# Kernel tuning notes

Hardware: AMD Instinct MI355X
Metric: run time of the kernel (lower is better)

## Reference

```python
import jax, jax.numpy as jnp
import numpy as np

S, D, H, HD, FF = 4096, 1024, 16, 64, 4096  # seq, d_embed, heads, head_dim, hidden
EPS = 1e-6  # flax LayerNorm default epsilon


def layer_norm(x, scale, bias):
    mu = jnp.mean(x, axis=-1, keepdims=True)
    var = jnp.var(x, axis=-1, keepdims=True)
    return (x - mu) * jax.lax.rsqrt(var + EPS) * scale + bias


def rope(x):
    # x: [S, H, HD]; standard half-split rotary embedding, base 10000
    half = x.shape[-1] // 2
    freq = 1.0 / (10000.0 ** (jnp.arange(half, dtype=x.dtype) / half))  # [half]
    ang = jnp.arange(x.shape[0], dtype=x.dtype)[:, None] * freq          # [S, half]
    cos = jnp.cos(ang)[:, None, :]
    sin = jnp.sin(ang)[:, None, :]
    x1, x2 = x[..., :half], x[..., half:]
    return jnp.concatenate([x1 * cos - x2 * sin, x2 * cos + x1 * sin], axis=-1)


def setup_inputs() -> dict:
    key = jax.random.key(0)
    ks = jax.random.split(key, 8)
    s = 0.02
    return {
        "x": jax.random.normal(ks[0], (S, D), jnp.float32),
        "ln1_scale": jnp.ones((D,), jnp.float32), "ln1_bias": jnp.zeros((D,), jnp.float32),
        "ln2_scale": jnp.ones((D,), jnp.float32), "ln2_bias": jnp.zeros((D,), jnp.float32),
        "Wq": jax.random.normal(ks[1], (D, H, HD), jnp.float32) * s, "bq": jnp.zeros((H, HD), jnp.float32),
        "Wk": jax.random.normal(ks[2], (D, H, HD), jnp.float32) * s, "bk": jnp.zeros((H, HD), jnp.float32),
        "Wv": jax.random.normal(ks[3], (D, H, HD), jnp.float32) * s, "bv": jnp.zeros((H, HD), jnp.float32),
        "Wo": jax.random.normal(ks[4], (H, HD, D), jnp.float32) * s, "bo": jnp.zeros((D,), jnp.float32),
        "W1": jax.random.normal(ks[5], (D, FF), jnp.float32) * s, "b1": jnp.zeros((FF,), jnp.float32),
        "W2": jax.random.normal(ks[6], (FF, D), jnp.float32) * s, "b2": jnp.zeros((D,), jnp.float32),
    }


def reference(x, ln1_scale, ln1_bias, ln2_scale, ln2_bias, Wq, bq, Wk, bk, Wv, bv, Wo, bo, W1, b1, W2, b2):
    # Pre-LN attention block with RoPE fused into QK scores
    y = layer_norm(x, ln1_scale, ln1_bias)
    q = jnp.einsum('sd,dhc->shc', y, Wq) + bq  # [S,H,HD]
    k = jnp.einsum('sd,dhc->shc', y, Wk) + bk
    v = jnp.einsum('sd,dhc->shc', y, Wv) + bv
    q = rope(q)
    k = rope(k)
    scores = jnp.einsum('qhc,khc->hqk', q, k) / jnp.sqrt(jnp.asarray(HD, x.dtype))  # [H,S,S]
    p = jax.nn.softmax(scores, axis=-1)
    o = jnp.einsum('hqk,khc->qhc', p, v)                # [S,H,HD]
    attn_out = jnp.einsum('qhc,hcd->qd', o, Wo) + bo    # [S,D]
    x = x + attn_out
    # Pre-LN GELU MLP block
    y = layer_norm(x, ln2_scale, ln2_bias)
    y = jax.nn.gelu(y @ W1 + b1, approximate=False)
    x = x + (y @ W2 + b2)
    return x
```

## Files before the change

### kernel.cpp

```cpp
#include <hip/hip_runtime.h>
#include <hip/hip_bf16.h>
#include <math.h>

using bf16 = __hip_bfloat16;
typedef __attribute__((ext_vector_type(8))) short short8;
typedef __attribute__((ext_vector_type(4))) short s16x4;
typedef __attribute__((ext_vector_type(4))) float f32x4;

constexpr int S = 4096, D = 1024, H = 16, HD = 64, FF = 4096;

static __device__ __forceinline__ float tof(bf16 v) { return __bfloat162float(v); }
static __device__ __forceinline__ bf16 tob(float v) { return __float2bfloat16(v); }
static __device__ __forceinline__ short tobs(float v) {
    bf16 h = __float2bfloat16(v);
    return *reinterpret_cast<short*>(&h);
}
static __device__ __forceinline__ unsigned pkbf16(float a, float b) {
    __hip_bfloat162 h = __float22bfloat162_rn(make_float2(a, b));
    return *reinterpret_cast<unsigned*>(&h);
}

#if __has_builtin(__builtin_amdgcn_exp2f)
#define EXP2(x) __builtin_amdgcn_exp2f(x)
#else
#define EXP2(x) exp2f(x)
#endif

static __device__ __forceinline__ f32x4 mfma16(short8 a, short8 b, f32x4 c) {
    return __builtin_amdgcn_mfma_f32_16x16x32_bf16(a, b, c, 0, 0, 0);
}
static __device__ __forceinline__ void stage16(const bf16* g, bf16* l) {
    __builtin_amdgcn_global_load_lds((__attribute__((address_space(1))) void*)g,
                                     (__attribute__((address_space(3))) void*)l, 16, 0, 0);
}

__global__ __launch_bounds__(256) void ln_kernel(const float* __restrict__ x,
                                                 const float* __restrict__ scale,
                                                 const float* __restrict__ bias,
                                                 bf16* __restrict__ y) {
    int row = blockIdx.x, t = threadIdx.x;
    const float* xr = x + (size_t)row * D;
    float v[4], s = 0.f, ss = 0.f;
#pragma unroll
    for (int i = 0; i < 4; ++i) {
        v[i] = xr[t + 256 * i];
        s += v[i]; ss += v[i] * v[i];
    }
    __shared__ float r0[256], r1[256];
    r0[t] = s; r1[t] = ss;
    __syncthreads();
    for (int off = 128; off; off >>= 1) {
        if (t < off) { r0[t] += r0[t + off]; r1[t] += r1[t + off]; }
        __syncthreads();
    }
    float mu  = r0[0] * (1.f / D);
    float var = r1[0] * (1.f / D) - mu * mu;
    float inv = rsqrtf(var + 1e-6f);
    bf16* yr = y + (size_t)row * D;
#pragma unroll
    for (int i = 0; i < 4; ++i) {
        int c = t + 256 * i;
        yr[c] = tob((v[i] - mu) * inv * scale[c] + bias[c]);
    }
}

__global__ __launch_bounds__(256) void wtrans_all(
    const float* __restrict__ Wq, const float* __restrict__ Wk,
    const float* __restrict__ Wv, const float* __restrict__ Wo,
    const float* __restrict__ W1, const float* __restrict__ W2,
    const float* __restrict__ bq, const float* __restrict__ bk,
    const float* __restrict__ bv,
    bf16* __restrict__ BTqkv, bf16* __restrict__ BTo,
    bf16* __restrict__ BT1, bf16* __restrict__ BT2, float* __restrict__ bqkv) {
    int id = blockIdx.x;
    if (id >= 12288) {
        int i = (id - 12288) * 256 + threadIdx.x;
        bqkv[i] = i < 1024 ? bq[i] : (i < 2048 ? bk[i - 1024] : bv[i - 2048]);
        return;
    }
    const float* W; bf16* dst; int K, N, local;
    if (id < 3072)      { int s = id >> 10; W = s == 0 ? Wq : (s == 1 ? Wk : Wv);
                          dst = BTqkv + (size_t)s * 1048576; K = 1024; N = 1024; local = id & 1023; }
    else if (id < 4096) { W = Wo; dst = BTo; K = 1024; N = 1024; local = id - 3072; }
    else if (id < 8192) { W = W1; dst = BT1; K = 1024; N = 4096; local = id - 4096; }
    else                { W = W2; dst = BT2; K = 4096; N = 1024; local = id - 8192; }
    int ls = (N == 4096) ? 7 : 5;
    int nt = (local & ((1 << ls) - 1)) << 5, kt = (local >> ls) << 5;
    __shared__ float t[32][33];
    int tid = threadIdx.x, r = tid >> 5, c = tid & 31;
#pragma unroll
    for (int p = 0; p < 4; ++p)
        t[r + p * 8][c] = W[(size_t)(kt + r + p * 8) * N + nt + c];
    __syncthreads();
#pragma unroll
    for (int p = 0; p < 4; ++p)
        dst[(size_t)(nt + r + p * 8) * K + kt + c] = tob(t[c][r + p * 8]);
}

#define EPI_RES  1
#define EPI_GELU 2
#define EPI_QKV  3

template <int EPI, int MT>
__global__ __launch_bounds__(256, MT == 128 ? 2 : 3) void gemm_bt(
    const bf16* __restrict__ A, const bf16* __restrict__ BT,
    const float* __restrict__ bias, const float* resid, void* out, void* out2,
    int M, int N, int K) {
    constexpr int NJ = (MT == 128) ? 4 : 2;
    __shared__ bf16 As[MT * 32];
    __shared__ bf16 Bs[128 * 32];
    const int tid = threadIdx.x;
    const int w = tid >> 6, lane = tid & 63;
    const int quad = lane >> 4, l16 = lane & 15;
    const int rowBase = blockIdx.y * MT, colBase = blockIdx.x * 128;
    const int wr = (MT == 128) ? (w >> 1) * 64 : 0;
    const int wc = (MT == 128) ? (w & 1) * 64 : w * 32;
    const int sr = lane >> 2, skb = (lane & 3) * 8;
    f32x4 acc[4][NJ] = {};
    for (int k0 = 0; k0 < K; k0 += 32) {
        __syncthreads();
        if (MT == 128) {
#pragma unroll
            for (int t = 0; t < 2; ++t) {
                int inst = w * 2 + t;
                int r = inst * 16 + sr;
                stage16(A  + (size_t)(rowBase + r) * K + k0 + skb, As + inst * 512);
                stage16(BT + (size_t)(colBase + r) * K + k0 + skb, Bs + inst * 512);
            }
        } else {
            stage16(A + (size_t)(rowBase + w * 16 + sr) * K + k0 + skb, As + w * 512);
#pragma unroll
            for (int t = 0; t < 2; ++t) {
                int inst = w + t * 4;
                stage16(BT + (size_t)(colBase + inst * 16 + sr) * K + k0 + skb, Bs + inst * 512);
            }
        }
        __syncthreads();
        const bf16* pa = As + (wr + l16) * 32 + quad * 8;
        const bf16* pb = Bs + (wc + l16) * 32 + quad * 8;
        short8 a[4], b[NJ];
#pragma unroll
        for (int i = 0; i < 4; ++i) a[i] = *(const short8*)(pa + i * 512);
#pragma unroll
        for (int j = 0; j < NJ; ++j) b[j] = *(const short8*)(pb + j * 512);
#pragma unroll
        for (int i = 0; i < 4; ++i)
#pragma unroll
            for (int j = 0; j < NJ; ++j) acc[i][j] = mfma16(a[i], b[j], acc[i][j]);
    }
    if (EPI == EPI_QKV) {
        bf16* QKVo = (bf16*)out;
        bf16* VTo  = (bf16*)out2;
        if (colBase >= 2048) {
#pragma unroll
            for (int j = 0; j < NJ; ++j) {
                int c = colBase + wc + j * 16 + l16;
                float bj = bias[c];
                size_t cc = (size_t)(c - 2048) * 4096;
#pragma unroll
                for (int i = 0; i < 4; ++i) {
                    int r0 = rowBase + wr + i * 16 + quad * 4;
                    s16x4 ov = {tobs(acc[i][j][0] + bj), tobs(acc[i][j][1] + bj),
                                tobs(acc[i][j][2] + bj), tobs(acc[i][j][3] + bj)};
                    *(s16x4*)(VTo + cc + r0) = ov;
                }
            }
        } else {
            const bool isq = colBase < 1024;
            const float qs = isq ? 0.125f * 1.44269504088896f : 1.f;
#pragma unroll
            for (int j2 = 0; j2 < 2; ++j2) {
                int dim = j2 * 16 + l16;
                float freq = __expf(-(float)dim * (9.210340371976184f / 32.f));
                int c1 = colBase + wc + j2 * 16 + l16, c2 = c1 + 32;
                float b1v = bias[c1], b2v = bias[c2];
#pragma unroll
                for (int i = 0; i < 4; ++i) {
#pragma unroll
                    for (int reg = 0; reg < 4; ++reg) {
                        int s = rowBase + wr + i * 16 + quad * 4 + reg;
                        float sn, cs;
                        sincosf((float)s * freq, &sn, &cs);
                        float x1 = acc[i][j2][reg] + b1v;
                        float x2 = acc[i][j2 + 2][reg] + b2v;
                        QKVo[(size_t)s * 3072 + c1] = tob((x1 * cs - x2 * sn) * qs);
                        QKVo[(size_t)s * 3072 + c2] = tob((x2 * cs + x1 * sn) * qs);
                    }
                }
            }
        }
    } else {
#pragma unroll
        for (int j = 0; j < NJ; ++j) {
            int c = colBase + wc + j * 16 + l16;
            float bj = bias[c];
#pragma unroll
            for (int i = 0; i < 4; ++i) {
                int r0 = rowBase + wr + i * 16 + quad * 4;
#pragma unroll
                for (int reg = 0; reg < 4; ++reg) {
                    size_t idx = (size_t)(r0 + reg) * N + c;
                    float val = acc[i][j][reg] + bj;
                    if (EPI == EPI_RES) {
                        ((float*)out)[idx] = val + resid[idx];
                    } else {
                        float g = 0.5f * val * (1.f + erff(val * 0.70710678118f));
                        ((bf16*)out)[idx] = tob(g);
                    }
                }
            }
        }
    }
}

__global__ __launch_bounds__(256, 4) void attn_kernel(const bf16* __restrict__ QKV,
                                                      const bf16* __restrict__ VT,
                                                      bf16* __restrict__ O) {
    const int h = blockIdx.x >> 6, qb = blockIdx.x & 63;
    const int w = threadIdx.x >> 6, lane = threadIdx.x & 63;
    const int quad = lane >> 4, l16 = lane & 15;
    const int q0w = qb * 64 + w * 16;
    const bf16* Qh = QKV + h * 64;
    const bf16* Kh = QKV + 1024 + h * 64;
    const bf16* Vh = VT + (size_t)h * 64 * 4096;

    __shared__ char smem[40960];
    bf16* Ks = (bf16*)(smem);
    bf16* Vs = (bf16*)(smem + 16384);
    char* Pb = smem + 32768 + w * 2048;

    const int sw = l16 & 7;
    const int rloc = lane >> 3, slot = lane & 7;
    const int schunk = (slot ^ rloc) * 8;
    const int row0 = 2 * w * 8 + rloc, row1 = (2 * w + 1) * 8 + rloc;
    const size_t kOff0 = (size_t)row0 * 3072 + schunk;
    const size_t kOff1 = (size_t)row1 * 3072 + schunk;
    const size_t vOff0 = (size_t)row0 * 4096 + schunk;
    const size_t vOff1 = (size_t)row1 * 4096 + schunk;

    short8 qf[2];
#pragma unroll
    for (int c = 0; c < 2; ++c)
        qf[c] = *(const short8*)(Qh + (size_t)(q0w + l16) * 3072 + c * 32 + quad * 8);

    const short ob = (l16 == 0) ? (short)0x3F80 : (short)0;
    const short8 ones8 = {ob, ob, ob, ob, ob, ob, ob, ob};

    f32x4 acc[4] = {};
    f32x4 accl = {};
    const f32x4 zero = {0.f, 0.f, 0.f, 0.f};

    auto stage = [&](int sel, int kt) {
        bf16* kd = Ks + sel * 4096 + 2 * w * 512;
        bf16* vd = Vs + sel * 4096 + 2 * w * 512;
        const bf16* kb = Kh + (size_t)kt * 3072;
        stage16(kb + kOff0, kd);
        stage16(kb + kOff1, kd + 512);
        stage16(Vh + vOff0 + kt, vd);
        stage16(Vh + vOff1 + kt, vd + 512);
    };
    auto compute = [&](int sel) {
        const bf16* Kt = Ks + sel * 4096;
        const bf16* Vt = Vs + sel * 4096;
        f32x4 st[4];
#pragma unroll
        for (int nt = 0; nt < 4; ++nt) {
            const bf16* kr = Kt + (nt * 16 + l16) * 64;
            short8 k0 = *(const short8*)(kr + ((quad ^ sw) * 8));
            short8 k1 = *(const short8*)(kr + (((quad + 4) ^ sw) * 8));
            st[nt] = mfma16(k1, qf[1], mfma16(k0, qf[0], zero));
        }
#pragma unroll
        for (int nt = 0; nt < 4; ++nt) {
            float e0 = EXP2(st[nt][0]), e1 = EXP2(st[nt][1]);
            float e2 = EXP2(st[nt][2]), e3 = EXP2(st[nt][3]);
            uint2 pk = {pkbf16(e0, e1), pkbf16(e2, e3)};
            *(uint2*)(Pb + l16 * 128 + (((nt * 2 + (quad >> 1)) ^ sw) * 16) + (quad & 1) * 8) = pk;
        }
        asm volatile("s_waitcnt lgkmcnt(0)" ::: "memory");
#pragma unroll
        for (int c = 0; c < 2; ++c) {
            short8 pB = *(const short8*)(Pb + l16 * 128 + (((c * 4 + quad) ^ sw) * 16));
            accl = mfma16(ones8, pB, accl);
#pragma unroll
            for (int vt = 0; vt < 4; ++vt) {
                short8 vf = *(const short8*)(Vt + (vt * 16 + l16) * 64 + (((c * 4 + quad) ^ sw) * 8));
                acc[vt] = mfma16(vf, pB, acc[vt]);
            }
        }
    };

    stage(0, 0);
    for (int kt = 0; kt < 4096; kt += 128) {
        __syncthreads();
        stage(1, kt + 64);
        compute(0);
        __syncthreads();
        if (kt + 128 < 4096) stage(0, kt + 128);
        compute(1);
    }

    float linv = 1.f / __shfl(accl[0], l16, 64);
#pragma unroll
    for (int vt = 0; vt < 4; ++vt) {
        s16x4 ov = {tobs(acc[vt][0] * linv), tobs(acc[vt][1] * linv),
                    tobs(acc[vt][2] * linv), tobs(acc[vt][3] * linv)};
        *(s16x4*)(O + (size_t)(q0w + l16) * 1024 + h * 64 + vt * 16 + quad * 4) = ov;
    }
}

extern "C" void kernel_launch(void* const* d_in, const int* in_sizes, int n_in,
                              void* d_out, int out_size, void* d_ws, size_t ws_size,
                              hipStream_t stream) {
    const float* x   = (const float*)d_in[0];
    const float* s1  = (const float*)d_in[1];
    const float* b1n = (const float*)d_in[2];
    const float* s2  = (const float*)d_in[3];
    const float* b2n = (const float*)d_in[4];
    const float* Wq  = (const float*)d_in[5];
    const float* bq  = (const float*)d_in[6];
    const float* Wk  = (const float*)d_in[7];
    const float* bk  = (const float*)d_in[8];
    const float* Wv  = (const float*)d_in[9];
    const float* bv  = (const float*)d_in[10];
    const float* Wo  = (const float*)d_in[11];
    const float* bo  = (const float*)d_in[12];
    const float* W1  = (const float*)d_in[13];
    const float* b1  = (const float*)d_in[14];
    const float* W2  = (const float*)d_in[15];
    const float* b2  = (const float*)d_in[16];

    char* ws = (char*)d_ws;
    bf16*  y     = (bf16*)(ws);
    bf16*  QKV   = (bf16*)(ws + (8ull  << 20));
    bf16*  o     = (bf16*)(ws + (32ull << 20));
    bf16*  hb    = (bf16*)(ws + (40ull << 20));
    bf16*  BTqkv = (bf16*)(ws + (40ull << 20));
    bf16*  BTo   = (bf16*)(ws + (46ull << 20));
    bf16*  VT    = (bf16*)(ws + (72ull << 20));
    bf16*  BT1   = (bf16*)(ws + (80ull << 20));
    bf16*  BT2   = (bf16*)(ws + (88ull << 20));
    float* bqkv  = (float*)(ws + (32ull << 20));
    float* x1    = (float*)d_out;

    wtrans_all<<<12300, 256, 0, stream>>>(Wq, Wk, Wv, Wo, W1, W2, bq, bk, bv,
                                          BTqkv, BTo, BT1, BT2, bqkv);

    ln_kernel<<<S, 256, 0, stream>>>(x, s1, b1n, y);

    gemm_bt<EPI_QKV, 128><<<dim3(24, 32), 256, 0, stream>>>(y, BTqkv, bqkv, nullptr, QKV, VT, S, 3072, D);

    attn_kernel<<<H * 64, 256, 0, stream>>>(QKV, VT, o);

    gemm_bt<EPI_RES, 64><<<dim3(8, 64), 256, 0, stream>>>(o, BTo, bo, x, x1, nullptr, S, D, D);

    ln_kernel<<<S, 256, 0, stream>>>(x1, s2, b2n, y);

    gemm_bt<EPI_GELU, 128><<<dim3(32, 32), 256, 0, stream>>>(y, BT1, b1, nullptr, hb, nullptr, S, FF, D);

    gemm_bt<EPI_RES, 64><<<dim3(8, 64), 256, 0, stream>>>(hb, BT2, b2, x1, d_out, nullptr, S, D, FF);
}
```

Measured before the change: 433.2 us.

## Split attention keys and FFN2 reduction into halves with merge kernels

The attention kernel now splits the key range into two halves per (head, 128-query block). Each wave handles two 16-query tiles, so every K/V fragment staged in shared memory is reused twice. It writes unnormalized fp32 partial outputs and row sums, which a new merge kernel adds and normalizes. The FFN2 GEMM gains a split-K mode over a z grid dimension that writes fp32 partials, and a second merge kernel sums them with the bias and residual. Q/K are also stored with a compact 2048 stride. The changes aim to raise parallelism and data reuse, but they add fp32 partial traffic and drop the attention kernel's double-buffered K/V staging.

```diff
diff --git a/kernel.cpp b/kernel.cpp
--- a/kernel.cpp
+++ b/kernel.cpp
@@ -100,12 +100,13 @@
 #define EPI_RES  1
 #define EPI_GELU 2
 #define EPI_QKV  3
+#define EPI_PART 4
 
 template <int EPI, int MT>
 __global__ __launch_bounds__(256, MT == 128 ? 2 : 3) void gemm_bt(
     const bf16* __restrict__ A, const bf16* __restrict__ BT,
     const float* __restrict__ bias, const float* resid, void* out, void* out2,
-    int M, int N, int K) {
+    int M, int N, int K, int kLen) {
     constexpr int NJ = (MT == 128) ? 4 : 2;
     __shared__ bf16 As[MT * 32];
     __shared__ bf16 Bs[128 * 32];
@@ -113,26 +114,27 @@
     const int w = tid >> 6, lane = tid & 63;
     const int quad = lane >> 4, l16 = lane & 15;
     const int rowBase = blockIdx.y * MT, colBase = blockIdx.x * 128;
+    const int kStart = blockIdx.z * kLen;
     const int wr = (MT == 128) ? (w >> 1) * 64 : 0;
     const int wc = (MT == 128) ? (w & 1) * 64 : w * 32;
     const int sr = lane >> 2, skb = (lane & 3) * 8;
     f32x4 acc[4][NJ] = {};
-    for (int k0 = 0; k0 < K; k0 += 32) {
+    for (int k0 = 0; k0 < kLen; k0 += 32) {
         __syncthreads();
         if (MT == 128) {
 #pragma unroll
             for (int t = 0; t < 2; ++t) {
                 int inst = w * 2 + t;
                 int r = inst * 16 + sr;
-                stage16(A  + (size_t)(rowBase + r) * K + k0 + skb, As + inst * 512);
-                stage16(BT + (size_t)(colBase + r) * K + k0 + skb, Bs + inst * 512);
+                stage16(A  + (size_t)(rowBase + r) * K + kStart + k0 + skb, As + inst * 512);
+                stage16(BT + (size_t)(colBase + r) * K + kStart + k0 + skb, Bs + inst * 512);
             }
         } else {
-            stage16(A + (size_t)(rowBase + w * 16 + sr) * K + k0 + skb, As + w * 512);
+            stage16(A + (size_t)(rowBase + w * 16 + sr) * K + kStart + k0 + skb, As + w * 512);
 #pragma unroll
             for (int t = 0; t < 2; ++t) {
                 int inst = w + t * 4;
-                stage16(BT + (size_t)(colBase + inst * 16 + sr) * K + k0 + skb, Bs + inst * 512);
+                stage16(BT + (size_t)(colBase + inst * 16 + sr) * K + kStart + k0 + skb, Bs + inst * 512);
             }
         }
         __syncthreads();
@@ -149,8 +151,8 @@
             for (int j = 0; j < NJ; ++j) acc[i][j] = mfma16(a[i], b[j], acc[i][j]);
     }
     if (EPI == EPI_QKV) {
-        bf16* QKVo = (bf16*)out;
-        bf16* VTo  = (bf16*)out2;
+        bf16* QKo = (bf16*)out;
+        bf16* VTo = (bf16*)out2;
         if (colBase >= 2048) {
 #pragma unroll
             for (int j = 0; j < NJ; ++j) {
@@ -183,8 +185,8 @@
                         sincosf((float)s * freq, &sn, &cs);
                         float x1 = acc[i][j2][reg] + b1v;
                         float x2 = acc[i][j2 + 2][reg] + b2v;
-                        QKVo[(size_t)s * 3072 + c1] = tob((x1 * cs - x2 * sn) * qs);
-                        QKVo[(size_t)s * 3072 + c2] = tob((x2 * cs + x1 * sn) * qs);
+                        QKo[(size_t)s * 2048 + c1] = tob((x1 * cs - x2 * sn) * qs);
+                        QKo[(size_t)s * 2048 + c2] = tob((x2 * cs + x1 * sn) * qs);
                     }
                 }
             }
@@ -193,7 +195,7 @@
 #pragma unroll
         for (int j = 0; j < NJ; ++j) {
             int c = colBase + wc + j * 16 + l16;
-            float bj = bias[c];
+            float bj = (EPI == EPI_PART) ? 0.f : bias[c];
 #pragma unroll
             for (int i = 0; i < 4; ++i) {
                 int r0 = rowBase + wr + i * 16 + quad * 4;
@@ -203,6 +205,8 @@
                     float val = acc[i][j][reg] + bj;
                     if (EPI == EPI_RES) {
                         ((float*)out)[idx] = val + resid[idx];
+                    } else if (EPI == EPI_PART) {
+                        ((float*)out)[(size_t)blockIdx.z * M * N + idx] = val;
                     } else {
                         float g = 0.5f * val * (1.f + erff(val * 0.70710678118f));
                         ((bf16*)out)[idx] = tob(g);
@@ -213,100 +217,131 @@
     }
 }
 
-__global__ __launch_bounds__(256, 4) void attn_kernel(const bf16* __restrict__ QKV,
+__global__ __launch_bounds__(256, 4) void attn_kernel(const bf16* __restrict__ QK,
                                                       const bf16* __restrict__ VT,
-                                                      bf16* __restrict__ O) {
-    const int h = blockIdx.x >> 6, qb = blockIdx.x & 63;
+                                                      float* __restrict__ Op,
+                                                      float* __restrict__ lp) {
+    const int bx = blockIdx.x;
+    const int h = bx >> 6, qb = (bx & 63) >> 1, kh = bx & 1;
     const int w = threadIdx.x >> 6, lane = threadIdx.x & 63;
     const int quad = lane >> 4, l16 = lane & 15;
-    const int q0w = qb * 64 + w * 16;
-    const bf16* Qh = QKV + h * 64;
-    const bf16* Kh = QKV + 1024 + h * 64;
+    const int q0w = qb * 128 + w * 32;
+    const bf16* Qh = QK + h * 64;
+    const bf16* Kh = QK + 1024 + h * 64;
     const bf16* Vh = VT + (size_t)h * 64 * 4096;
 
-    __shared__ char smem[40960];
+    __shared__ char smem[32768];
     bf16* Ks = (bf16*)(smem);
-    bf16* Vs = (bf16*)(smem + 16384);
-    char* Pb = smem + 32768 + w * 2048;
+    bf16* Vs = (bf16*)(smem + 8192);
+    char* Pw = smem + 16384 + w * 4096;
 
     const int sw = l16 & 7;
     const int rloc = lane >> 3, slot = lane & 7;
     const int schunk = (slot ^ rloc) * 8;
-    const int row0 = 2 * w * 8 + rloc, row1 = (2 * w + 1) * 8 + rloc;
-    const size_t kOff0 = (size_t)row0 * 3072 + schunk;
-    const size_t kOff1 = (size_t)row1 * 3072 + schunk;
-    const size_t vOff0 = (size_t)row0 * 4096 + schunk;
-    const size_t vOff1 = (size_t)row1 * 4096 + schunk;
-
-    short8 qf[2];
-#pragma unroll
-    for (int c = 0; c < 2; ++c)
-        qf[c] = *(const short8*)(Qh + (size_t)(q0w + l16) * 3072 + c * 32 + quad * 8);
+    const int row0 = w * 16 + rloc, row1 = w * 16 + 8 + rloc;
+
+    short8 qf[2][2];
+#pragma unroll
+    for (int qt = 0; qt < 2; ++qt)
+#pragma unroll
+        for (int c = 0; c < 2; ++c)
+            qf[qt][c] = *(const short8*)(Qh + (size_t)(q0w + qt * 16 + l16) * 2048 + c * 32 + quad * 8);
 
     const short ob = (l16 == 0) ? (short)0x3F80 : (short)0;
     const short8 ones8 = {ob, ob, ob, ob, ob, ob, ob, ob};
 
-    f32x4 acc[4] = {};
-    f32x4 accl = {};
+    f32x4 acc[4][2] = {};
+    f32x4 accl[2] = {};
     const f32x4 zero = {0.f, 0.f, 0.f, 0.f};
-
-    auto stage = [&](int sel, int kt) {
-        bf16* kd = Ks + sel * 4096 + 2 * w * 512;
-        bf16* vd = Vs + sel * 4096 + 2 * w * 512;
-        const bf16* kb = Kh + (size_t)kt * 3072;
-        stage16(kb + kOff0, kd);
-        stage16(kb + kOff1, kd + 512);
-        stage16(Vh + vOff0 + kt, vd);
-        stage16(Vh + vOff1 + kt, vd + 512);
-    };
-    auto compute = [&](int sel) {
-        const bf16* Kt = Ks + sel * 4096;
-        const bf16* Vt = Vs + sel * 4096;
-        f32x4 st[4];
+    const int ktBeg = kh * 2048;
+
+    for (int kt = 0; kt < 2048; kt += 64) {
+        const int ktA = ktBeg + kt;
+        __syncthreads();
+        stage16(Kh + (size_t)(ktA + row0) * 2048 + schunk, Ks + w * 1024);
+        stage16(Kh + (size_t)(ktA + row1) * 2048 + schunk, Ks + w * 1024 + 512);
+        stage16(Vh + (size_t)row0 * 4096 + ktA + schunk, Vs + w * 1024);
+        stage16(Vh + (size_t)row1 * 4096 + ktA + schunk, Vs + w * 1024 + 512);
+        __syncthreads();
+
+        f32x4 st[4][2];
 #pragma unroll
         for (int nt = 0; nt < 4; ++nt) {
-            const bf16* kr = Kt + (nt * 16 + l16) * 64;
+            const bf16* kr = Ks + (nt * 16 + l16) * 64;
             short8 k0 = *(const short8*)(kr + ((quad ^ sw) * 8));
             short8 k1 = *(const short8*)(kr + (((quad + 4) ^ sw) * 8));
-            st[nt] = mfma16(k1, qf[1], mfma16(k0, qf[0], zero));
+#pragma unroll
+            for (int qt = 0; qt < 2; ++qt)
+                st[nt][qt] = mfma16(k1, qf[qt][1], mfma16(k0, qf[qt][0], zero));
         }
 #pragma unroll
-        for (int nt = 0; nt < 4; ++nt) {
-            float e0 = EXP2(st[nt][0]), e1 = EXP2(st[nt][1]);
-            float e2 = EXP2(st[nt][2]), e3 = EXP2(st[nt][3]);
-            uint2 pk = {pkbf16(e0, e1), pkbf16(e2, e3)};
-            *(uint2*)(Pb + l16 * 128 + (((nt * 2 + (quad >> 1)) ^ sw) * 16) + (quad & 1) * 8) = pk;
+        for (int nt = 0; nt < 4; ++nt)
+#pragma unroll
+            for (int qt = 0; qt < 2; ++qt) {
+                float e0 = EXP2(st[nt][qt][0]), e1 = EXP2(st[nt][qt][1]);
+                float e2 = EXP2(st[nt][qt][2]), e3 = EXP2(st[nt][qt][3]);
+                uint2 pk = {pkbf16(e0, e1), pkbf16(e2, e3)};
+                *(uint2*)(Pw + (qt * 16 + l16) * 128 +
+                          (((nt * 2 + (quad >> 1)) ^ sw) * 16) + (quad & 1) * 8) = pk;
+            }
+        asm volatile("s_waitcnt lgkmcnt(0)" ::: "memory");
+#pragma unroll
+        for (int c = 0; c < 2; ++c) {
+            short8 pB[2];
+#pragma unroll
+            for (int qt = 0; qt < 2; ++qt) {
+                pB[qt] = *(const short8*)(Pw + (qt * 16 + l16) * 128 + (((c * 4 + quad) ^ sw) * 16));
+                accl[qt] = mfma16(ones8, pB[qt], accl[qt]);
+            }
+#pragma unroll
+            for (int vt = 0; vt < 4; ++vt) {
+                short8 vf = *(const short8*)(Vs + (vt * 16 + l16) * 64 + (((c * 4 + quad) ^ sw) * 8));
+#pragma unroll
+                for (int qt = 0; qt < 2; ++qt)
+                    acc[vt][qt] = mfma16(vf, pB[qt], acc[vt][qt]);
+            }
         }
-        asm volatile("s_waitcnt lgkmcnt(0)" ::: "memory");
-#pragma unroll
-        for (int c = 0; c < 2; ++c) {
-            short8 pB = *(const short8*)(Pb + l16 * 128 + (((c * 4 + quad) ^ sw) * 16));
-            accl = mfma16(ones8, pB, accl);
-#pragma unroll
-            for (int vt = 0; vt < 4; ++vt) {
-                short8 vf = *(const short8*)(Vt + (vt * 16 + l16) * 64 + (((c * 4 + quad) ^ sw) * 8));
-                acc[vt] = mfma16(vf, pB, acc[vt]);
-            }
-        }
-    };
-
-    stage(0, 0);
-    for (int kt = 0; kt < 4096; kt += 128) {
-        __syncthreads();
-        stage(1, kt + 64);
-        compute(0);
-        __syncthreads();
-        if (kt + 128 < 4096) stage(0, kt + 128);
-        compute(1);
-    }
-
-    float linv = 1.f / __shfl(accl[0], l16, 64);
-#pragma unroll
-    for (int vt = 0; vt < 4; ++vt) {
-        s16x4 ov = {tobs(acc[vt][0] * linv), tobs(acc[vt][1] * linv),
-                    tobs(acc[vt][2] * linv), tobs(acc[vt][3] * linv)};
-        *(s16x4*)(O + (size_t)(q0w + l16) * 1024 + h * 64 + vt * 16 + quad * 4) = ov;
-    }
+    }
+    float* Oz = Op + (size_t)kh * (4096 * 1024);
+#pragma unroll
+    for (int qt = 0; qt < 2; ++qt) {
+        int q = q0w + qt * 16 + l16;
+#pragma unroll
+        for (int vt = 0; vt < 4; ++vt)
+            *(f32x4*)(Oz + (size_t)q * 1024 + h * 64 + vt * 16 + quad * 4) = acc[vt][qt];
+        if (quad == 0) lp[kh * 65536 + h * 4096 + q] = accl[qt][0];
+    }
+}
+
+__global__ __launch_bounds__(256) void merge_attn(const float* __restrict__ Op,
+                                                  const float* __restrict__ lp,
+                                                  bf16* __restrict__ o) {
+    int i = blockIdx.x * 256 + threadIdx.x;
+    int d4 = i * 4;
+    int s = d4 >> 10, d = d4 & 1023, h = d >> 6;
+    f32x4 a = *(const f32x4*)(Op + d4 + (size_t)s * 0);
+    f32x4 b = *(const f32x4*)(Op + 4194304 + d4);
+    float linv = 1.f / (lp[h * 4096 + s] + lp[65536 + h * 4096 + s]);
+    s16x4 ov = {tobs(a[0] + b[0]) , 0, 0, 0};
+    ov[0] = tobs((a[0] + b[0]) * linv);
+    ov[1] = tobs((a[1] + b[1]) * linv);
+    ov[2] = tobs((a[2] + b[2]) * linv);
+    ov[3] = tobs((a[3] + b[3]) * linv);
+    *(s16x4*)(o + d4) = ov;
+}
+
+__global__ __launch_bounds__(256) void merge_ffn2(const float* __restrict__ pb,
+                                                  const float* __restrict__ b2,
+                                                  float* __restrict__ out) {
+    int i = blockIdx.x * 256 + threadIdx.x;
+    int d4 = i * 4, c = d4 & 1023;
+    f32x4 a = *(const f32x4*)(pb + d4);
+    f32x4 b = *(const f32x4*)(pb + 4194304 + d4);
+    f32x4 r = *(const f32x4*)(out + d4);
+    f32x4 bb = *(const f32x4*)(b2 + c);
+    f32x4 v = {a[0] + b[0] + r[0] + bb[0], a[1] + b[1] + r[1] + bb[1],
+               a[2] + b[2] + r[2] + bb[2], a[3] + b[3] + r[3] + bb[3]};
+    *(f32x4*)(out + d4) = v;
 }
 
 extern "C" void kernel_launch(void* const* d_in, const int* in_sizes, int n_in,
@@ -331,32 +366,37 @@
     const float* b2  = (const float*)d_in[16];
 
     char* ws = (char*)d_ws;
-    bf16*  y     = (bf16*)(ws);
-    bf16*  QKV   = (bf16*)(ws + (8ull  << 20));
-    bf16*  o     = (bf16*)(ws + (32ull << 20));
-    bf16*  hb    = (bf16*)(ws + (40ull << 20));
-    bf16*  BTqkv = (bf16*)(ws + (40ull << 20));
-    bf16*  BTo   = (bf16*)(ws + (46ull << 20));
-    bf16*  VT    = (bf16*)(ws + (72ull << 20));
-    bf16*  BT1   = (bf16*)(ws + (80ull << 20));
-    bf16*  BT2   = (bf16*)(ws + (88ull << 20));
-    float* bqkv  = (float*)(ws + (32ull << 20));
-    float* x1    = (float*)d_out;
+    bf16*  y    = (bf16*)(ws);
+    bf16*  QK   = (bf16*)(ws + (8ull  << 20));
+    bf16*  BTo  = (bf16*)(ws + (24ull << 20));
+    float* lp   = (float*)(ws + (26ull << 20));
+    float* bqkv = (float*)(ws + (27ull << 20));
+    bf16*  o    = (bf16*)(ws + (32ull << 20));
+    bf16*  hb   = (bf16*)(ws + (40ull << 20));
+    bf16*  BTqkv= (bf16*)(ws + (40ull << 20));
+    float* Op   = (float*)(ws + (40ull << 20));
+    bf16*  VT   = (bf16*)(ws + (72ull << 20));
+    bf16*  BT1  = (bf16*)(ws + (80ull << 20));
+    bf16*  BT2  = (bf16*)(ws + (88ull << 20));
+    float* pb   = (float*)(ws);
+    float* x1   = (float*)d_out;
 
     wtrans_all<<<12300, 256, 0, stream>>>(Wq, Wk, Wv, Wo, W1, W2, bq, bk, bv,
                                           BTqkv, BTo, BT1, BT2, bqkv);
 
     ln_kernel<<<S, 256, 0, stream>>>(x, s1, b1n, y);
 
-    gemm_bt<EPI_QKV, 128><<<dim3(24, 32), 256, 0, stream>>>(y, BTqkv, bqkv, nullptr, QKV, VT, S, 3072, D);
-
-    attn_kernel<<<H * 64, 256, 0, stream>>>(QKV, VT, o);
-
-    gemm_bt<EPI_RES, 64><<<dim3(8, 64), 256, 0, stream>>>(o, BTo, bo, x, x1, nullptr, S, D, D);
+    gemm_bt<EPI_QKV, 128><<<dim3(24, 32), 256, 0, stream>>>(y, BTqkv, bqkv, nullptr, QK, VT, S, 3072, D, D);
+
+    attn_kernel<<<H * 64, 256, 0, stream>>>(QK, VT, Op, lp);
+    merge_attn<<<4096, 256, 0, stream>>>(Op, lp, o);
+
+    gemm_bt<EPI_RES, 64><<<dim3(8, 64), 256, 0, stream>>>(o, BTo, bo, x, x1, nullptr, S, D, D, D);
 
     ln_kernel<<<S, 256, 0, stream>>>(x1, s2, b2n, y);
 
-    gemm_bt<EPI_GELU, 128><<<dim3(32, 32), 256, 0, stream>>>(y, BT1, b1, nullptr, hb, nullptr, S, FF, D);
-
-    gemm_bt<EPI_RES, 64><<<dim3(8, 64), 256, 0, stream>>>(hb, BT2, b2, x1, d_out, nullptr, S, D, FF);
-}
+    gemm_bt<EPI_GELU, 128><<<dim3(32, 32), 256, 0, stream>>>(y, BT1, b1, nullptr, hb, nullptr, S, FF, D, D);
+
+    gemm_bt<EPI_PART, 64><<<dim3(8, 64, 2), 256, 0, stream>>>(hb, BT2, b2, nullptr, pb, nullptr, S, D, FF, 2048);
+    merge_ffn2<<<4096, 256, 0, stream>>>(pb, b2, x1);
+}
```

Result: faster. 422.9 us (-2.4%).
